# Kernel tuning notes

Hardware: AMD Instinct MI355X
Metric: run time of the kernel (lower is better)

## Reference

```python
import jax, jax.numpy as jnp
import numpy as np

FUTURE = 64  # future_information_samples; equals Dense output_size


def setup_inputs() -> dict:
    key = jax.random.key(0)
    ks = jax.random.split(key, 5)
    B, T, F, H = 128, 512, 64, 512
    sF = 1.0 / np.sqrt(F)
    sH = 1.0 / np.sqrt(H)
    return {
        "x": jax.random.normal(ks[0], (B, T, F), dtype=jnp.float32),
        "W": jax.random.normal(ks[1], (F, 4 * H), dtype=jnp.float32) * sF,
        "U": jax.random.normal(ks[2], (H, 4 * H), dtype=jnp.float32) * sH,
        "b": jnp.zeros((4 * H,), dtype=jnp.float32),
        "Wd": jax.random.normal(ks[3], (H, FUTURE), dtype=jnp.float32) * sH,
        "bd": jnp.zeros((FUTURE,), dtype=jnp.float32),
    }


def _lstm_last_h(x, W, U, b):
    # Keras LSTM, activation='relu' (cell/output act), recurrent_activation='sigmoid'.
    # Gate order in Keras kernels: i, f, c(g), o. Only the last hidden state is
    # consumed downstream (x[:, -1, :]), so we carry (h, c) through a scan.
    B = x.shape[0]
    H = U.shape[0]
    x_proj = jnp.einsum("btf,fk->btk", x, W) + b  # precompute input GEMM: [B,T,4H]
    x_tm = jnp.swapaxes(x_proj, 0, 1)  # time-major [T,B,4H]

    def step(carry, zx):
        h, c = carry
        z = zx + h @ U  # [B,4H]
        i, f, g, o = jnp.split(z, 4, axis=-1)
        i = jax.nn.sigmoid(i)
        f = jax.nn.sigmoid(f)
        g = jax.nn.relu(g)
        o = jax.nn.sigmoid(o)
        c = f * c + i * g
        h = o * jax.nn.relu(c)
        return (h, c), None

    h0 = jnp.zeros((B, H), dtype=x.dtype)
    c0 = jnp.zeros((B, H), dtype=x.dtype)
    (h_last, _), _ = jax.lax.scan(step, (h0, c0), x_tm)
    return h_last


def reference(x, W, U, b, Wd, bd):
    h = _lstm_last_h(x, W, U, b)          # [B,H]
    y = h @ Wd + bd                        # [B,FUTURE] (linear Dense)
    return y.reshape(-1, FUTURE, 1)        # [B,FUTURE,1]
```

## Files before the change

kernel.cpp:

```cpp
#include <hip/hip_runtime.h>
#include <stdint.h>

#define Bq   128
#define Tq   512
#define Fq   64
#define Hq   512
#define G4q  2048
#define FUTq 64


typedef __attribute__((ext_vector_type(8))) short bfrag_t;
typedef __attribute__((ext_vector_type(4))) float accf_t;
typedef __attribute__((ext_vector_type(4))) float f4_t;
typedef __attribute__((ext_vector_type(4))) unsigned int u32x4;

static __device__ __forceinline__ accf_t mfma16(uint4 a, uint4 b, accf_t acc) {
  return __builtin_amdgcn_mfma_f32_16x16x32_bf16(
      __builtin_bit_cast(bfrag_t, a), __builtin_bit_cast(bfrag_t, b), acc, 0, 0, 0);
}

static __device__ __forceinline__ void pack2(float f0, float f1, uint32_t& h, uint32_t& l) {
  uint32_t b0 = __float_as_uint(f0), b1 = __float_as_uint(f1);
  h = (b0 >> 16) | (b1 & 0xffff0000u);
  float r0 = f0 - __uint_as_float(b0 & 0xffff0000u);
  float r1 = f1 - __uint_as_float(b1 & 0xffff0000u);
  l = (__float_as_uint(r0) >> 16) | (__float_as_uint(r1) & 0xffff0000u);
}

static __device__ __forceinline__ float sigmoidf_(float v) {
  return __fdividef(1.0f, 1.0f + __expf(-v));
}

#define LD16(dst, base, IMM)                                                \
  asm volatile("global_load_dwordx4 %0, %1, off offset:" IMM " sc0 sc1"     \
               : "=v"(dst) : "v"(base) : "memory")
static __device__ __forceinline__ void st16_cc(void* p, u32x4 v) {
  asm volatile("global_store_dwordx4 %0, %1, off sc0 sc1" :: "v"(p), "v"(v) : "memory");
}
static __device__ __forceinline__ void stf_cc(void* p, float v) {
  asm volatile("global_store_dword %0, %1, off sc0 sc1" :: "v"(p), "v"(v) : "memory");
}
static __device__ __forceinline__ void wait_vm0() {
  asm volatile("s_waitcnt vmcnt(0)" ::: "memory");
  __builtin_amdgcn_sched_barrier(0);
}

static __device__ __forceinline__ void poll1(uint32_t* f, uint32_t tgt) {
  int guard = 0;
  while (__hip_atomic_load(f, __ATOMIC_RELAXED, __HIP_MEMORY_SCOPE_AGENT) < tgt) {
    __builtin_amdgcn_s_sleep(1);
    if (++guard > (1 << 23)) return;
  }
}

__global__ __launch_bounds__(256, 1) void lstm_persist(
    const float* __restrict__ x, const float* __restrict__ W,
    const float* __restrict__ U, const float* __restrict__ bias_v,
    const float* __restrict__ Wd, const float* __restrict__ bd,
    uint32_t* __restrict__ hbuf,
    uint32_t* __restrict__ prod,
    float* __restrict__ hfin,
    float* __restrict__ out)
{
  const int wg  = blockIdx.x;
  const int mg  = wg & 7;
  const int ng  = wg >> 3;
  const int tid = threadIdx.x;
  const int wv  = tid >> 6;
  const int l   = tid & 63;
  const int c   = l & 15;
  const int h4  = l >> 4;
  const int gate = c & 3;
  const int unit = ng * 16 + wv * 4 + (c >> 2);
  const int srccol = gate * 512 + unit;

  __shared__ float lds[128][65];
  __shared__ uint32_t stg[2][16][16];
  __shared__ uint4 fragH[16 * 64];
  __shared__ uint4 fragL[16 * 64];

  uint4 Bhi[16], Blo[16];
  const int srow = tid >> 2, sg = tid & 3;
  #pragma unroll
  for (int tb = 0; tb < 4; ++tb) {
    __syncthreads();
    #pragma unroll
    for (int p = 0; p < 2; ++p) {
      const int kl = p * 64 + srow;
      const float* src = U + (size_t)(tb * 128 + kl) * G4q + sg * 512 + ng * 16;
      #pragma unroll
      for (int q = 0; q < 4; ++q) {
        f4_t vv = *(const f4_t*)(src + q * 4);
        #pragma unroll
        for (int e = 0; e < 4; ++e) {
          int uu = q * 4 + e;
          lds[kl][(uu >> 2) * 16 + (uu & 3) * 4 + sg] = vv[e];
        }
      }
    }
    __syncthreads();
    #pragma unroll
    for (int k2 = 0; k2 < 4; ++k2) {
      const int kk = tb * 4 + k2;
      uint32_t wh[4], wl[4];
      #pragma unroll
      for (int jp = 0; jp < 4; ++jp) {
        const int kloc = k2 * 32 + h4 * 8 + jp * 2;
        pack2(lds[kloc][wv * 16 + c], lds[kloc + 1][wv * 16 + c], wh[jp], wl[jp]);
      }
      Bhi[kk] = make_uint4(wh[0], wh[1], wh[2], wh[3]);
      Blo[kk] = make_uint4(wl[0], wl[1], wl[2], wl[3]);
    }
  }

  uint4 Wh[2], Wl[2];
  __syncthreads();
  {
    const float* src = W + (size_t)srow * G4q + sg * 512 + ng * 16;
    #pragma unroll
    for (int q = 0; q < 4; ++q) {
      f4_t vv = *(const f4_t*)(src + q * 4);
      #pragma unroll
      for (int e = 0; e < 4; ++e) {
        int uu = q * 4 + e;
        lds[srow][(uu >> 2) * 16 + (uu & 3) * 4 + sg] = vv[e];
      }
    }
  }
  __syncthreads();
  #pragma unroll
  for (int kk = 0; kk < 2; ++kk) {
    uint32_t wh[4], wl[4];
    #pragma unroll
    for (int jp = 0; jp < 4; ++jp) {
      const int kloc = kk * 32 + h4 * 8 + jp * 2;
      pack2(lds[kloc][wv * 16 + c], lds[kloc + 1][wv * 16 + c], wh[jp], wl[jp]);
    }
    Wh[kk] = make_uint4(wh[0], wh[1], wh[2], wh[3]);
    Wl[kk] = make_uint4(wl[0], wl[1], wl[2], wl[3]);
  }
  __syncthreads();

  const float bval = bias_v[srccol];
  float cst[4] = {0.f, 0.f, 0.f, 0.f};

  const float* xrow = x + (size_t)(mg * 16 + c) * Tq * Fq + h4 * 8;
  const char*  hbb  = (const char*)hbuf;
  const size_t rowoff = (size_t)(mg * 16 + c) * 2048 + h4 * 32;
  uint32_t* fb = prod + mg * 32;

  for (int t = 0; t < Tq; ++t) {
    const int pb = t & 1;

    accf_t accA = {bval, bval, bval, bval};
    accf_t accB = {0.f, 0.f, 0.f, 0.f};
    accf_t accC = {0.f, 0.f, 0.f, 0.f};
    {
      const float* xp = xrow + (size_t)t * Fq;
      #pragma unroll
      for (int kk = 0; kk < 2; ++kk) {
        f4_t xa = *(const f4_t*)(xp + kk * 32);
        f4_t xb = *(const f4_t*)(xp + kk * 32 + 4);
        uint32_t xh[4], xl[4];
        pack2(xa[0], xa[1], xh[0], xl[0]);
        pack2(xa[2], xa[3], xh[1], xl[1]);
        pack2(xb[0], xb[1], xh[2], xl[2]);
        pack2(xb[2], xb[3], xh[3], xl[3]);
        uint4 XH = make_uint4(xh[0], xh[1], xh[2], xh[3]);
        uint4 XL = make_uint4(xl[0], xl[1], xl[2], xl[3]);
        accA = mfma16(XH, Wh[kk], accA);
        accB = mfma16(XL, Wh[kk], accB);
        accC = mfma16(XH, Wl[kk], accC);
      }
    }

    if (wv == 0) {
      int guard = 0;
      for (;;) {
        uint32_t v = __hip_atomic_load(&fb[l & 31], __ATOMIC_RELAXED,
                                       __HIP_MEMORY_SCOPE_AGENT);
        if (!__ballot(v < (uint32_t)t)) break;
        __builtin_amdgcn_s_sleep(1);
        if (++guard > (1 << 23)) break;
      }
    }
    __syncthreads();

    {
      const char* hp2 = hbb + (size_t)pb * 262144 + rowoff + wv * 512;
      uint4 q0, q1, q2, q3, q4, q5, q6, q7;
      LD16(q0, hp2, "0");   LD16(q1, hp2, "16");
      LD16(q2, hp2, "128"); LD16(q3, hp2, "144");
      LD16(q4, hp2, "256"); LD16(q5, hp2, "272");
      LD16(q6, hp2, "384"); LD16(q7, hp2, "400");
      wait_vm0();
      uint4 qs[8] = {q0, q1, q2, q3, q4, q5, q6, q7};
      #pragma unroll
      for (int jj = 0; jj < 4; ++jj) {
        uint4 a = qs[2 * jj], b = qs[2 * jj + 1];
        uint4 ahf, alf;
        ahf.x = __builtin_amdgcn_perm(a.y, a.x, 0x05040100u);
        ahf.y = __builtin_amdgcn_perm(a.w, a.z, 0x05040100u);
        ahf.z = __builtin_amdgcn_perm(b.y, b.x, 0x05040100u);
        ahf.w = __builtin_amdgcn_perm(b.w, b.z, 0x05040100u);
        alf.x = __builtin_amdgcn_perm(a.y, a.x, 0x07060302u);
        alf.y = __builtin_amdgcn_perm(a.w, a.z, 0x07060302u);
        alf.z = __builtin_amdgcn_perm(b.y, b.x, 0x07060302u);
        alf.w = __builtin_amdgcn_perm(b.w, b.z, 0x07060302u);
        fragH[(wv * 4 + jj) * 64 + l] = ahf;
        fragL[(wv * 4 + jj) * 64 + l] = alf;
      }
    }
    __syncthreads();

    #pragma unroll
    for (int j = 0; j < 16; ++j) {
      uint4 ah = fragH[j * 64 + l];
      uint4 al = fragL[j * 64 + l];
      accA = mfma16(ah, Bhi[j], accA);
      accB = mfma16(al, Bhi[j], accB);
      accC = mfma16(ah, Blo[j], accC);
    }

    uint32_t word_out = 0;
    #pragma unroll
    for (int r = 0; r < 4; ++r) {
      float zr = accA[r] + accB[r] + accC[r];
      float s1 = __shfl_xor(zr, 1);
      float s2 = __shfl_xor(zr, 2);
      float s3 = __shfl_xor(zr, 3);
      const bool b0 = (gate & 1), b1 = (gate & 2);
      float t01a = b0 ? s1 : zr, t23a = b0 ? s3 : s2;
      float iv = b1 ? t23a : t01a;
      float gv = b1 ? t01a : t23a;
      float t01b = b0 ? zr : s1, t23b = b0 ? s2 : s3;
      float fv = b1 ? t23b : t01b;
      float ov = b1 ? t01b : t23b;
      float si = sigmoidf_(iv);
      float sf = sigmoidf_(fv);
      float so = sigmoidf_(ov);
      float cn = sf * cst[r] + si * fmaxf(gv, 0.f);
      cst[r] = cn;
      float hn = so * fmaxf(cn, 0.f);

      uint32_t hb = __float_as_uint(hn);
      uint32_t hi16 = hb >> 16;
      float res = hn - __uint_as_float(hb & 0xffff0000u);
      uint32_t lo16 = __float_as_uint(res) >> 16;
      uint32_t word = hi16 | (lo16 << 16);
      if (gate == r) word_out = word;
      if (t == Tq - 1 && gate == r)
        stf_cc(hfin + (size_t)(mg * 16 + h4 * 4 + r) * Hq + unit, hn);
    }
    stg[pb][h4 * 4 + gate][wv * 4 + (c >> 2)] = word_out;

    if (t == Tq - 1) wait_vm0();
    __syncthreads();

    if (wv == 1) {
      const int pn = pb ^ 1;
      u32x4 v = *(const u32x4*)&stg[pb][l >> 2][(l & 3) * 4];
      char* sp = (char*)hbuf + (size_t)pn * 262144 +
                 (size_t)(mg * 16 + (l >> 2)) * 2048 + ng * 64 + (l & 3) * 16;
      st16_cc(sp, v);
      asm volatile("s_waitcnt vmcnt(0)" ::: "memory");
      if (l == 0)
        __hip_atomic_store(&prod[mg * 32 + ng], (uint32_t)(t + 1),
                           __ATOMIC_RELAXED, __HIP_MEMORY_SCOPE_AGENT);
    }
  }

  if (wg < 32) {
    const int mgy = wg >> 2;
    if (tid < 32) poll1(&prod[mgy * 32 + tid], (uint32_t)Tq);
    __syncthreads();
    float* lflat = &lds[0][0];
    {
      const int r = tid >> 6, o = (tid & 63) * 8;
      const char* src = (const char*)(hfin + (size_t)(wg * 4 + r) * Hq + o);
      uint4 a, b;
      LD16(a, src, "0");
      LD16(b, src, "16");
      wait_vm0();
      *(uint4*)(lflat + r * 512 + o) = a;
      *(uint4*)(lflat + r * 512 + o + 4) = b;
    }
    __syncthreads();
    const int r = tid >> 6, j = tid & 63;
    const float* hr = lflat + r * 512;
    float acc = bd[j];
    #pragma unroll 8
    for (int k = 0; k < Hq; ++k)
      acc = fmaf(hr[k], Wd[(size_t)k * FUTq + j], acc);
    out[(wg * 4 + r) * FUTq + j] = acc;
  }
}

extern "C" void kernel_launch(void* const* d_in, const int* in_sizes, int n_in,
                              void* d_out, int out_size, void* d_ws, size_t ws_size,
                              hipStream_t stream) {
  (void)in_sizes; (void)n_in; (void)out_size; (void)ws_size;
  const float* x  = (const float*)d_in[0];
  const float* W  = (const float*)d_in[1];
  const float* U  = (const float*)d_in[2];
  const float* b  = (const float*)d_in[3];
  const float* Wd = (const float*)d_in[4];
  const float* bd = (const float*)d_in[5];

  uint32_t* hbuf = (uint32_t*)d_ws;
  uint32_t* prod = (uint32_t*)((char*)d_ws + 524288);
  float*    hfin = (float*)((char*)d_ws + 528384);

  (void)hipMemsetAsync(d_ws, 0, 525312, stream);

  hipLaunchKernelGGL(lstm_persist, dim3(256), dim3(256), 0, stream,
                     x, W, U, b, Wd, bd, hbuf, prod, hfin, (float*)d_out);
}
```

Before: 2.215 ms.

## Replace per-step flag polling with parity tags embedded in hidden-state data

Each hidden-state word now carries a parity bit in its low-residual bf16 half, and consumer waves poll the h buffer directly until every loaded word shows the expected parity. This drops the separate producer flag store, its vmcnt wait before the flag, and the workgroup barrier after polling, so the data load doubles as the readiness check. The cost is one bit of precision in the residual part of h, a second memset to seed the odd buffer with 0xFF, and all waves spinning on global loads instead of just one.

```diff
diff --git a/kernel.cpp b/kernel.cpp
--- a/kernel.cpp
+++ b/kernel.cpp
@@ -147,10 +147,19 @@
   const float* xrow = x + (size_t)(mg * 16 + c) * Tq * Fq + h4 * 8;
   const char*  hbb  = (const char*)hbuf;
   const size_t rowoff = (size_t)(mg * 16 + c) * 2048 + h4 * 32;
-  uint32_t* fb = prod + mg * 32;
 
   for (int t = 0; t < Tq; ++t) {
     const int pb = t & 1;
+    const uint32_t tb16 = (((uint32_t)t >> 1) & 1u) << 16;
+
+    const char* hp2 = hbb + (size_t)pb * 262144 + rowoff + wv * 512;
+    uint4 q0, q1, q2, q3, q4, q5, q6, q7;
+#define LOAD8 do {                                                   \
+      LD16(q0, hp2, "0");   LD16(q1, hp2, "16");                     \
+      LD16(q2, hp2, "128"); LD16(q3, hp2, "144");                    \
+      LD16(q4, hp2, "256"); LD16(q5, hp2, "272");                    \
+      LD16(q6, hp2, "384"); LD16(q7, hp2, "400"); } while (0)
+    LOAD8;
 
     accf_t accA = {bval, bval, bval, bval};
     accf_t accB = {0.f, 0.f, 0.f, 0.f};
@@ -174,26 +183,22 @@
       }
     }
 
-    if (wv == 0) {
+    {
       int guard = 0;
       for (;;) {
-        uint32_t v = __hip_atomic_load(&fb[l & 31], __ATOMIC_RELAXED,
-                                       __HIP_MEMORY_SCOPE_AGENT);
-        if (!__ballot(v < (uint32_t)t)) break;
+        wait_vm0();
+        uint32_t mm = ((q0.x ^ tb16) | (q1.x ^ tb16) | (q2.x ^ tb16) |
+                       (q3.x ^ tb16) | (q4.x ^ tb16) | (q5.x ^ tb16) |
+                       (q6.x ^ tb16) | (q7.x ^ tb16)) & 0x10000u;
+        if (!__ballot(mm != 0)) break;
         __builtin_amdgcn_s_sleep(1);
-        if (++guard > (1 << 23)) break;
-      }
-    }
-    __syncthreads();
+        if (++guard > (1 << 22)) break;
+        LOAD8;
+      }
+    }
+#undef LOAD8
 
     {
-      const char* hp2 = hbb + (size_t)pb * 262144 + rowoff + wv * 512;
-      uint4 q0, q1, q2, q3, q4, q5, q6, q7;
-      LD16(q0, hp2, "0");   LD16(q1, hp2, "16");
-      LD16(q2, hp2, "128"); LD16(q3, hp2, "144");
-      LD16(q4, hp2, "256"); LD16(q5, hp2, "272");
-      LD16(q6, hp2, "384"); LD16(q7, hp2, "400");
-      wait_vm0();
       uint4 qs[8] = {q0, q1, q2, q3, q4, q5, q6, q7};
       #pragma unroll
       for (int jj = 0; jj < 4; ++jj) {
@@ -259,13 +264,14 @@
 
     if (wv == 1) {
       const int pn = pb ^ 1;
+      const uint32_t ntag = (((uint32_t)(t + 1) >> 1) & 1u) << 16;
       u32x4 v = *(const u32x4*)&stg[pb][l >> 2][(l & 3) * 4];
+      v.x = (v.x & ~0x10000u) | ntag;
       char* sp = (char*)hbuf + (size_t)pn * 262144 +
                  (size_t)(mg * 16 + (l >> 2)) * 2048 + ng * 64 + (l & 3) * 16;
       st16_cc(sp, v);
-      asm volatile("s_waitcnt vmcnt(0)" ::: "memory");
-      if (l == 0)
-        __hip_atomic_store(&prod[mg * 32 + ng], (uint32_t)(t + 1),
+      if (t == Tq - 1 && l == 0)
+        __hip_atomic_store(&prod[mg * 32 + ng], (uint32_t)Tq,
                            __ATOMIC_RELAXED, __HIP_MEMORY_SCOPE_AGENT);
     }
   }
@@ -311,7 +317,9 @@
   uint32_t* prod = (uint32_t*)((char*)d_ws + 524288);
   float*    hfin = (float*)((char*)d_ws + 528384);
 
-  (void)hipMemsetAsync(d_ws, 0, 525312, stream);
+  (void)hipMemsetAsync(d_ws, 0, 262144, stream);
+  (void)hipMemsetAsync((char*)d_ws + 262144, 0xFF, 262144, stream);
+  (void)hipMemsetAsync((char*)d_ws + 524288, 0, 1024, stream);
 
   hipLaunchKernelGGL(lstm_persist, dim3(256), dim3(256), 0, stream,
                      x, W, U, b, Wd, bd, hbuf, prod, hfin, (float*)d_out);
```

Result: slower. 3.070 ms (+38.6%).
